# Kernel tuning notes

Hardware: AMD Instinct MI355X
Metric: run time of the kernel (lower is better)

The kernel has to match this reference:

```python
import jax, jax.numpy as jnp
import numpy as np
from functools import partial

INF = 1e10


def _softmin(a, b, c, gamma):
    # soft-min via -gamma * logsumexp(-x/gamma), numerically stable
    z = jnp.stack([a, b, c], axis=0) * (-1.0 / gamma)
    return -gamma * jax.nn.logsumexp(z, axis=0)


def rkd_sdtw(x, gamma):
    """Pairwise soft-DTW distances between all sequence pairs in the batch.

    x: [B, T, D] -> returns [B, B].
    """
    B, T, D = x.shape
    # pairwise squared-euclidean cost: C[a,b,t,s] = ||x[a,t]-x[b,s]||^2
    xn = jnp.sum(x * x, axis=-1)                      # [B, T]
    dot = jnp.einsum('atd,bsd->abts', x, x)           # [B, B, T, T]
    C = xn[:, None, :, None] + xn[None, :, None, :] - 2.0 * dot
    P = B * B
    C = C.reshape(P, T, T)

    idx = jnp.arange(T)

    def shift(r):  # r[i] -> r[i-1], pad INF at i=0
        return jnp.concatenate([jnp.full((P, 1), INF, r.dtype), r[:, :-1]], axis=1)

    def step(carry, d):
        r2, r1 = carry                                # diagonals d-2, d-1: [P, T]
        j = d - idx
        valid = (j >= 0) & (j < T)
        jc = jnp.clip(j, 0, T - 1)
        c_diag = C[:, idx, jc]                        # [P, T] cost on diagonal d
        up = shift(r1)        # R[i-1, j]
        left = r1             # R[i, j-1]
        diag = shift(r2)      # R[i-1, j-1]
        smin = _softmin(up, left, diag, gamma)
        smin = jnp.where(d == 0, 0.0, smin)           # R[0,0] = C[0,0]
        r = jnp.where(valid[None, :], c_diag + smin, INF)
        return (r1, r), None

    init = jnp.full((P, T), INF, C.dtype)
    (_, r_last), _ = jax.lax.scan(step, (init, init), jnp.arange(2 * T - 1))
    return r_last[:, T - 1].reshape(B, B)


def _smooth_l1(pred, target):
    d = pred - target
    ad = jnp.abs(d)
    return jnp.mean(jnp.where(ad < 1.0, 0.5 * d * d, ad - 0.5))


def setup_inputs() -> dict:
    key = jax.random.key(0)
    k1, k2 = jax.random.split(key)
    B, T, D = 32, 96, 128
    student = jax.random.normal(k1, (B, T, D), dtype=jnp.float32)
    teacher = jax.random.normal(k2, (B, T, D), dtype=jnp.float32)
    gamma = jnp.float32(1.0)
    return {"student": student, "teacher": teacher, "gamma": gamma}


def reference(student, teacher, gamma):
    # teacher branch computed under no_grad in torch -> stop_gradient here
    dtw_t = rkd_sdtw(teacher, gamma)
    dtw_t = dtw_t / jnp.mean(dtw_t)
    dtw_t = jax.lax.stop_gradient(dtw_t)

    dtw_s = rkd_sdtw(student, gamma)
    dtw_s = dtw_s / jnp.mean(dtw_s)
    return _smooth_l1(dtw_s, dtw_t)
```

## Files before the change

kernel.cpp:

```cpp
#include <hip/hip_runtime.h>


constexpr int TT = 96;
constexpr int DD = 128;
constexpr int BB = 32;
constexpr int NP = BB * BB;
constexpr int NPAIR = BB * (BB + 1) / 2;
constexpr int NPROB = 2 * NPAIR;
constexpr int CSZ = TT * TT;
constexpr float FINF = 1e10f;
constexpr float LOG2E = 1.4426950408889634f;
constexpr float LN2 = 0.6931471805599453f;

__device__ __forceinline__ int tri_base(int a) {
  return a * BB - (a * (a - 1)) / 2;
}
__device__ __forceinline__ void tri_decode(int pr, int& a, int& b) {
  a = (int)((65.0f - sqrtf(4225.0f - 8.0f * (float)pr)) * 0.5f);
  while (tri_base(a + 1) <= pr) ++a;
  while (tri_base(a) > pr) --a;
  b = a + (pr - tri_base(a));
}
__device__ __forceinline__ int diag_base(int d) {
  return (d <= 95) ? ((d * (d + 1)) >> 1)
                   : 4656 + (((d - 96) * (287 - d)) >> 1);
}
__device__ __forceinline__ float smin2(float u, float lf, float dg) {
  float m = fmaxf(fmaxf(u, lf), dg);
  float s = __builtin_amdgcn_exp2f(u - m) + __builtin_amdgcn_exp2f(lf - m)
          + __builtin_amdgcn_exp2f(dg - m);
  return m + __builtin_amdgcn_logf(s);
}

__global__ void xn_kernel(const float* __restrict__ xs,
                          const float* __restrict__ xt,
                          float* __restrict__ xn) {
  int idx = blockIdx.x * 256 + threadIdx.x;
  if (idx >= 2 * BB * TT) return;
  int which = idx / (BB * TT);
  int row = idx - which * (BB * TT);
  const float* x = which ? xt : xs;
  const float4* xv = reinterpret_cast<const float4*>(x + (size_t)row * DD);
  float acc = 0.f;
#pragma unroll
  for (int k = 0; k < DD / 4; ++k) {
    float4 v = xv[k];
    acc = fmaf(v.x, v.x, acc);
    acc = fmaf(v.y, v.y, acc);
    acc = fmaf(v.z, v.z, acc);
    acc = fmaf(v.w, v.w, acc);
  }
  xn[idx] = acc;
}

__global__ __launch_bounds__(256)
void csq_kernel(const float* __restrict__ xs,
                const float* __restrict__ xt,
                const float* __restrict__ xn,
                const float* __restrict__ gptr,
                float* __restrict__ Cd) {
  __shared__ __align__(16) float Cs[CSZ];
  __shared__ float xna[TT];
  __shared__ float xnb[TT];

  const int pr = blockIdx.x;
  int a, b;
  tri_decode(pr, a, b);
  const int w = blockIdx.y;
  const float* x = w ? xt : xs;
  const float* xnw = xn + w * (BB * TT);
  const float* xa = x + (size_t)a * TT * DD;
  const float* xb = x + (size_t)b * TT * DD;
  const int tid = threadIdx.x;

  if (tid < TT) {
    xna[tid] = xnw[a * TT + tid];
    xnb[tid] = xnw[b * TT + tid];
  }

  float4* sa = reinterpret_cast<float4*>(Cs);
  float4* sb = sa + TT * 9;

  const int wv = tid >> 6;
  const int lane = tid & 63;
  const int tx = (lane & 7) + (wv & 1) * 8;
  const int ty = (lane >> 3) + (wv >> 1) * 8;
  const int t0 = ty * 6, s0 = tx * 6;

  float acc[6][6];
#pragma unroll
  for (int r = 0; r < 6; ++r)
#pragma unroll
    for (int c = 0; c < 6; ++c) acc[r][c] = 0.f;

  const float4* ga = reinterpret_cast<const float4*>(xa);
  const float4* gb = reinterpret_cast<const float4*>(xb);

  for (int d0 = 0; d0 < 4; ++d0) {
    __syncthreads();
#pragma unroll
    for (int it = 0; it < 3; ++it) {
      int idx = tid + it * 256;
      int t = idx >> 3, k4 = idx & 7;
      int slot = (k4 + (t / 6)) & 7;
      sa[t * 9 + slot] = ga[t * 32 + d0 * 8 + k4];
      sb[t * 9 + slot] = gb[t * 32 + d0 * 8 + k4];
    }
    __syncthreads();
#pragma unroll
    for (int k4 = 0; k4 < 8; ++k4) {
      float4 av4[6], bv4[6];
      const int sA = (k4 + ty) & 7;
      const int sB = (k4 + tx) & 7;
#pragma unroll
      for (int r = 0; r < 6; ++r)
        av4[r] = sa[(t0 + r) * 9 + sA];
#pragma unroll
      for (int c = 0; c < 6; ++c)
        bv4[c] = sb[(s0 + c) * 9 + sB];
#pragma unroll
      for (int r = 0; r < 6; ++r)
#pragma unroll
        for (int c = 0; c < 6; ++c) {
          acc[r][c] = fmaf(av4[r].x, bv4[c].x, acc[r][c]);
          acc[r][c] = fmaf(av4[r].y, bv4[c].y, acc[r][c]);
          acc[r][c] = fmaf(av4[r].z, bv4[c].z, acc[r][c]);
          acc[r][c] = fmaf(av4[r].w, bv4[c].w, acc[r][c]);
        }
    }
  }
  __syncthreads();
  const float rg2 = -LOG2E / gptr[0];
#pragma unroll
  for (int r = 0; r < 6; ++r) {
    float xr = xna[t0 + r];
#pragma unroll
    for (int c = 0; c < 6; ++c) {
      float cv = xr + xnb[s0 + c] - 2.0f * acc[r][c];
      Cs[(t0 + r) * TT + (s0 + c)] = cv * rg2;
    }
  }
  __syncthreads();

  const size_t qb = (size_t)(w * NPAIR + pr) * CSZ;
  for (int d = wv; d < 2 * TT - 1; d += 4) {
    int s = d <= 95 ? 0 : d - 95;
    int len = d <= 95 ? d + 1 : 191 - d;
    int base = diag_base(d);
    if (lane < len) {
      int i = s + lane;
      Cd[qb + base + lane] = Cs[i * TT + (d - i)];
    }
    if (len > 64 && lane < len - 64) {
      int i = s + 64 + lane;
      Cd[qb + base + 64 + lane] = Cs[i * TT + (d - i)];
    }
  }
}

#define ST_R(d, qa, qb) do {                                             \
    float cA = qa, cB = qb;                                              \
    { int dn = (d) + 4;                                                  \
      if (dn <= 190) { int nb = diag_base(dn);                           \
        qa = cb[nb + l]; qb = cb[nb + 64 + l]; } }                       \
    float rA1 = __shfl(A1, lm1), rB1 = __shfl(B1, lm1);                  \
    float upA = l0 ? NEGI : rA1;                                         \
    float dgA = l0 ? NEGI : pA1;                                         \
    float upB = l0 ? rA1 : rB1;                                          \
    float dgB = l0 ? pA1 : pB1;                                          \
    float nA = cA + smin2(upA, A1, dgA);                                 \
    float nB = cB + smin2(upB, B1, dgB);                                 \
    A2 = A1; B2 = B1;                                                    \
    A1 = (l < (d) + 1) ? nA : NEGI;                                      \
    B1 = (64 + l < (d) + 1) ? nB : NEGI;                                 \
    pA1 = rA1; pB1 = rB1;                                                \
  } while (0)

#define ST_RN(d, qa, qb) do {       \
    float cA = qa;                                                       \
    { int dn = (d) + 4;                                                  \
      if (dn <= 190) { int nb = diag_base(dn);                           \
        qa = cb[nb + l]; qb = cb[nb + 64 + l]; } }                       \
    float rA1 = __shfl(A1, lm1);                                         \
    float upA = l0 ? NEGI : rA1;                                         \
    float dgA = l0 ? NEGI : pA1;                                         \
    float nA = cA + smin2(upA, A1, dgA);                                 \
    A2 = A1;                                                             \
    A1 = (l < (d) + 1) ? nA : NEGI;                                      \
    pA1 = rA1;                                                           \
  } while (0)

#define ST_F(d, qa, qb) do {                                             \
    float cA = qa, cB = qb;                                              \
    { int dn = (d) + 4;                                                  \
      if (dn <= 190) { int nb = diag_base(dn); qa = cb[nb + l];          \
        if (dn <= 128) qb = cb[nb + 64 + l]; } }                         \
    float rA1 = __shfl(A1, lp1), rB1 = __shfl(B1, lp1);                  \
    float lfA = l63 ? rB1 : rA1;                                         \
    float dgA = l63 ? pB1 : pA1;                                         \
    float nA = cA + smin2(A1, lfA, dgA);                                 \
    float nB = cB + smin2(B1, rB1, pB1);                                 \
    A1 = (l < 191 - (d)) ? nA : NEGI;                                    \
    B1 = (64 + l < 191 - (d)) ? nB : NEGI;                               \
    pA1 = rA1; pB1 = rB1;                                                \
  } while (0)

#define ST_FN(d, qa, qb) do {     \
    float cA = qa;                                                       \
    { int dn = (d) + 4;                                                  \
      if (dn <= 190) { int nb = diag_base(dn); qa = cb[nb + l]; } }      \
    float rA1 = __shfl(A1, lp1);                                         \
    float lfA = l63 ? NEGI : rA1;                                        \
    float dgA = l63 ? NEGI : pA1;                                        \
    float nA = cA + smin2(A1, lfA, dgA);                                 \
    A1 = (l < 191 - (d)) ? nA : NEGI;                                    \
    pA1 = rA1;                                                           \
  } while (0)

__global__ __launch_bounds__(64)
void dp_kernel(const float* __restrict__ Cd,
               const float* __restrict__ gptr,
               float* __restrict__ dtw) {
  const int q = blockIdx.x;
  const int l = threadIdx.x;
  const float gamma = gptr[0];
  const float rg2 = -LOG2E / gamma;
  const float NEGI = FINF * rg2;
  const float* __restrict__ cb = Cd + (size_t)q * CSZ;
  const int lp1 = (l + 1) & 63, lm1 = (l + 63) & 63;
  const bool l0 = (l == 0), l63 = (l == 63);

  float q0A, q0B, q1A, q1B, q2A, q2B, q3A, q3B;
  {
    int b1 = diag_base(1), b2 = diag_base(2), b3 = diag_base(3), b4 = diag_base(4);
    q0A = cb[b1 + l]; q0B = cb[b1 + 64 + l];
    q1A = cb[b2 + l]; q1B = cb[b2 + 64 + l];
    q2A = cb[b3 + l]; q2B = cb[b3 + 64 + l];
    q3A = cb[b4 + l]; q3B = cb[b4 + 64 + l];
  }

  float A1 = l0 ? cb[0] : NEGI;
  float B1 = NEGI, A2 = NEGI, B2 = NEGI;
  float pA1 = NEGI, pB1 = NEGI;

  for (int g = 0; g < 15; ++g) {
    int d = 1 + g * 4;
    ST_RN(d,     q0A, q0B);
    ST_RN(d + 1, q1A, q1B);
    ST_RN(d + 2, q2A, q2B);
    ST_RN(d + 3, q3A, q3B);
  }
  ST_RN(61, q0A, q0B);
  ST_RN(62, q1A, q1B);
  ST_RN(63, q2A, q2B);

  ST_R(64, q3A, q3B);
  for (int g = 0; g < 7; ++g) {
    int d = 65 + g * 4;
    ST_R(d,     q0A, q0B);
    ST_R(d + 1, q1A, q1B);
    ST_R(d + 2, q2A, q2B);
    ST_R(d + 3, q3A, q3B);
  }
  ST_R(93, q0A, q0B);
  ST_R(94, q1A, q1B);
  ST_R(95, q2A, q2B);

  {
    float cA = q3A, cB = q3B;
    int nb = diag_base(100);
    q3A = cb[nb + l]; q3B = cb[nb + 64 + l];
    float rA1 = __shfl(A1, lp1), rB1 = __shfl(B1, lp1);
    float lfA = l63 ? rB1 : rA1;
    float lfB = rB1;
    float nA = cA + smin2(A1, lfA, A2);
    float nB = cB + smin2(B1, lfB, B2);
    A1 = (l < 95) ? nA : NEGI;
    B1 = (64 + l < 95) ? nB : NEGI;
    pA1 = rA1; pB1 = rB1;
  }

  for (int g = 0; g < 8; ++g) {
    int d = 97 + g * 4;
    ST_F(d,     q0A, q0B);
    ST_F(d + 1, q1A, q1B);
    ST_F(d + 2, q2A, q2B);
    ST_F(d + 3, q3A, q3B);
  }
  for (int g = 0; g < 15; ++g) {
    int d = 129 + g * 4;
    ST_FN(d,     q0A, q0B);
    ST_FN(d + 1, q1A, q1B);
    ST_FN(d + 2, q2A, q2B);
    ST_FN(d + 3, q3A, q3B);
  }
  ST_FN(189, q0A, q0B);
  ST_FN(190, q1A, q1B);

  if (l0) {
    int w = q >= NPAIR ? 1 : 0;
    int pr = q - w * NPAIR;
    int a, b;
    tri_decode(pr, a, b);
    float v = A1 * (-gamma * LN2);
    dtw[w * NP + a * BB + b] = v;
    dtw[w * NP + b * BB + a] = v;
  }
}

__global__ __launch_bounds__(256)
void sdtw_fused_kernel(const float* __restrict__ xs,
                       const float* __restrict__ xt,
                       const float* __restrict__ xn,
                       const float* __restrict__ gptr,
                       float* __restrict__ dtw) {
  __shared__ __align__(16) float Cs[TT * TT];
  __shared__ float xna[TT];
  __shared__ float xnb[TT];

  const int pr = blockIdx.x;
  int a, b;
  tri_decode(pr, a, b);
  const int w = blockIdx.y;
  const float* x = w ? xt : xs;
  const float* xnw = xn + w * (BB * TT);
  const float* xa = x + (size_t)a * TT * DD;
  const float* xb = x + (size_t)b * TT * DD;
  const int tid = threadIdx.x;

  if (tid < TT) {
    xna[tid] = xnw[a * TT + tid];
    xnb[tid] = xnw[b * TT + tid];
  }
  constexpr int SROW = 36;
  float* xa_s = Cs;
  float* xb_s = Cs + TT * SROW;
  const int wv = tid >> 6;
  const int lane = tid & 63;
  const int tx = (lane & 7) + (wv & 1) * 8;
  const int ty = (lane >> 3) + (wv >> 1) * 8;
  const int t0 = ty * 6, s0 = tx * 6;
  float acc[6][6];
#pragma unroll
  for (int r = 0; r < 6; ++r)
#pragma unroll
    for (int c = 0; c < 6; ++c) acc[r][c] = 0.f;
  for (int d0 = 0; d0 < DD; d0 += 32) {
    __syncthreads();
    const float4* ga = reinterpret_cast<const float4*>(xa + d0);
    const float4* gb = reinterpret_cast<const float4*>(xb + d0);
    float4* sa = reinterpret_cast<float4*>(xa_s);
    float4* sb = reinterpret_cast<float4*>(xb_s);
#pragma unroll
    for (int it = 0; it < 3; ++it) {
      int idx = tid + it * 256;
      int t = idx >> 3, k4 = idx & 7;
      sa[t * (SROW / 4) + k4] = ga[t * (DD / 4) + k4];
      sb[t * (SROW / 4) + k4] = gb[t * (DD / 4) + k4];
    }
    __syncthreads();
#pragma unroll
    for (int k4 = 0; k4 < 8; ++k4) {
      float4 av4[6], bv4[6];
#pragma unroll
      for (int r = 0; r < 6; ++r)
        av4[r] = reinterpret_cast<const float4*>(xa_s + (t0 + r) * SROW)[k4];
#pragma unroll
      for (int c = 0; c < 6; ++c)
        bv4[c] = reinterpret_cast<const float4*>(xb_s + (s0 + c) * SROW)[k4];
#pragma unroll
      for (int r = 0; r < 6; ++r)
#pragma unroll
        for (int c = 0; c < 6; ++c) {
          acc[r][c] = fmaf(av4[r].x, bv4[c].x, acc[r][c]);
          acc[r][c] = fmaf(av4[r].y, bv4[c].y, acc[r][c]);
          acc[r][c] = fmaf(av4[r].z, bv4[c].z, acc[r][c]);
          acc[r][c] = fmaf(av4[r].w, bv4[c].w, acc[r][c]);
        }
    }
  }
  __syncthreads();
#pragma unroll
  for (int r = 0; r < 6; ++r) {
    float xr = xna[t0 + r];
#pragma unroll
    for (int c = 0; c < 6; ++c)
      Cs[(t0 + r) * TT + (s0 + c)] = xr + xnb[s0 + c] - 2.0f * acc[r][c];
  }
  __syncthreads();
  if (tid >= 64) return;

  const float gamma = gptr[0];
  const float rg = -1.0f / gamma;
  const int lm1 = (lane + 63) & 63;
  float A1 = FINF, B1 = FINF, A2 = FINF, B2 = FINF;
  for (int d = 0; d < 2 * TT - 1; ++d) {
    int jA = d - lane;
    bool vA = (jA >= 0) && (jA < TT);
    float cA = Cs[vA ? lane * TT + jA : 0];
    int iB = 64 + lane;
    int jB = d - iB;
    bool vB = (lane < 32) && (jB >= 0) && (jB < TT);
    float cB = Cs[vB ? iB * TT + jB : 0];
    float rA1 = __shfl(A1, lm1);
    float rB1 = __shfl(B1, lm1);
    float rA2 = __shfl(A2, lm1);
    float rB2 = __shfl(B2, lm1);
    const bool l0 = (lane == 0);
    float upA = l0 ? FINF : rA1;
    float dgA = l0 ? FINF : rA2;
    float upB = l0 ? rA1 : rB1;
    float dgB = l0 ? rA2 : rB2;
    float z0 = upA * rg, z1 = A1 * rg, z2 = dgA * rg;
    float m = fmaxf(fmaxf(z0, z1), z2);
    float s = expf(z0 - m) + expf(z1 - m) + expf(z2 - m);
    float sminA = -gamma * (m + logf(s));
    if (d == 0) sminA = 0.f;
    float y0 = upB * rg, y1 = B1 * rg, y2 = dgB * rg;
    float mb = fmaxf(fmaxf(y0, y1), y2);
    float sb2 = expf(y0 - mb) + expf(y1 - mb) + expf(y2 - mb);
    float sminB = -gamma * (mb + logf(sb2));
    float nA = vA ? cA + sminA : FINF;
    float nB = vB ? cB + sminB : FINF;
    A2 = A1; B2 = B1; A1 = nA; B1 = nB;
  }
  if (lane == 31) {
    float v = B1;
    dtw[w * NP + a * BB + b] = v;
    dtw[w * NP + b * BB + a] = v;
  }
}

__global__ void reduce_kernel(const float* __restrict__ dtw,
                              float* __restrict__ out) {
  __shared__ double sh[256];
  const int tid = threadIdx.x;
  double ss = 0, st = 0;
  for (int k = tid; k < NP; k += 256) {
    ss += (double)dtw[k];
    st += (double)dtw[NP + k];
  }
  sh[tid] = ss; __syncthreads();
  for (int o = 128; o > 0; o >>= 1) { if (tid < o) sh[tid] += sh[tid + o]; __syncthreads(); }
  double sum_s = sh[0]; __syncthreads();
  sh[tid] = st; __syncthreads();
  for (int o = 128; o > 0; o >>= 1) { if (tid < o) sh[tid] += sh[tid + o]; __syncthreads(); }
  double sum_t = sh[0]; __syncthreads();

  float mean_s = (float)(sum_s / NP);
  float mean_t = (float)(sum_t / NP);

  double acc = 0;
  for (int k = tid; k < NP; k += 256) {
    float pred = dtw[k] / mean_s;
    float targ = dtw[NP + k] / mean_t;
    float d = pred - targ;
    float ad = fabsf(d);
    float v = ad < 1.f ? 0.5f * d * d : ad - 0.5f;
    acc += (double)v;
  }
  sh[tid] = acc; __syncthreads();
  for (int o = 128; o > 0; o >>= 1) { if (tid < o) sh[tid] += sh[tid + o]; __syncthreads(); }
  if (tid == 0) out[0] = (float)(sh[0] / NP);
}

extern "C" void kernel_launch(void* const* d_in, const int* in_sizes, int n_in,
                              void* d_out, int out_size, void* d_ws, size_t ws_size,
                              hipStream_t stream) {
  const float* student = (const float*)d_in[0];
  const float* teacher = (const float*)d_in[1];
  const float* gamma   = (const float*)d_in[2];
  float* ws = (float*)d_ws;

  const size_t cd_floats = (size_t)NPROB * CSZ;
  const size_t need = (cd_floats + 2 * NP + 2 * BB * TT) * sizeof(float);

  if (ws_size >= need) {
    float* Cd  = ws;
    float* dtw = ws + cd_floats;
    float* xnb = dtw + 2 * NP;
    xn_kernel<<<24, 256, 0, stream>>>(student, teacher, xnb);
    csq_kernel<<<dim3(NPAIR, 2), 256, 0, stream>>>(student, teacher, xnb, gamma, Cd);
    dp_kernel<<<NPROB, 64, 0, stream>>>(Cd, gamma, dtw);
    reduce_kernel<<<1, 256, 0, stream>>>(dtw, (float*)d_out);
  } else {
    float* dtw = ws;
    float* xnb = ws + 2 * NP;
    xn_kernel<<<24, 256, 0, stream>>>(student, teacher, xnb);
    sdtw_fused_kernel<<<dim3(NPAIR, 2), 256, 0, stream>>>(student, teacher, xnb, gamma, dtw);
    reduce_kernel<<<1, 256, 0, stream>>>(dtw, (float*)d_out);
  }
}
```

Measured before the change: 93.22 us.

## Redundantly compute neighbor DP cells to move shuffles off the critical path

Each lane now also computes a ghost copy of its neighbor's cell on the anti-diagonal, loading the extra cost values. The shuffle that fetches the neighbor's value is issued after the update and consumed one step later, so cross-lane latency overlaps the next step's compute. In exchange the soft-min arithmetic and global loads per step roughly double, and the phase transitions get more complex bookkeeping.

```diff
diff --git a/kernel.cpp b/kernel.cpp
--- a/kernel.cpp
+++ b/kernel.cpp
@@ -158,63 +158,81 @@
   }
 }
 
-#define ST_R(d, qa, qb) do {                                             \
-    float cA = qa, cB = qb;                                              \
-    { int dn = (d) + 4;                                                  \
-      if (dn <= 190) { int nb = diag_base(dn);                           \
-        qa = cb[nb + l]; qb = cb[nb + 64 + l]; } }                       \
-    float rA1 = __shfl(A1, lm1), rB1 = __shfl(B1, lm1);                  \
-    float upA = l0 ? NEGI : rA1;                                         \
-    float dgA = l0 ? NEGI : pA1;                                         \
-    float upB = l0 ? rA1 : rB1;                                          \
-    float dgB = l0 ? pA1 : pB1;                                          \
-    float nA = cA + smin2(upA, A1, dgA);                                 \
-    float nB = cB + smin2(upB, B1, dgB);                                 \
-    A2 = A1; B2 = B1;                                                    \
-    A1 = (l < (d) + 1) ? nA : NEGI;                                      \
-    B1 = (64 + l < (d) + 1) ? nB : NEGI;                                 \
-    pA1 = rA1; pB1 = rB1;                                                \
+#define PREF(dn, sA, sG, sB, sH) do {                                    \
+    if ((dn) <= 190) {                                                   \
+      int nb = diag_base(dn);                                            \
+      int iA = nb + l;                 if (iA > CSZ - 1) iA = CSZ - 1;   \
+      sA = cb[iA];                                                       \
+      int iG = ((dn) <= 95) ? (nb + l - 1) : (nb + l + 1);               \
+      if (iG > CSZ - 1) iG = CSZ - 1;                                    \
+      sG = cb[iG];                                                       \
+      if ((dn) >= 63 && (dn) <= 128) {                                   \
+        int iB = nb + 64 + l;          if (iB > CSZ - 1) iB = CSZ - 1;   \
+        sB = cb[iB];                                                     \
+        int iH = ((dn) <= 95) ? (nb + 63 + l) : (nb + 65 + l);           \
+        if (iH > CSZ - 1) iH = CSZ - 1;                                  \
+        sH = cb[iH];                                                     \
+      }                                                                  \
+    }                                                                    \
   } while (0)
 
-#define ST_RN(d, qa, qb) do {       \
-    float cA = qa;                                                       \
-    { int dn = (d) + 4;                                                  \
-      if (dn <= 190) { int nb = diag_base(dn);                           \
-        qa = cb[nb + l]; qb = cb[nb + 64 + l]; } }                       \
-    float rA1 = __shfl(A1, lm1);                                         \
-    float upA = l0 ? NEGI : rA1;                                         \
-    float dgA = l0 ? NEGI : pA1;                                         \
-    float nA = cA + smin2(upA, A1, dgA);                                 \
-    A2 = A1;                                                             \
-    A1 = (l < (d) + 1) ? nA : NEGI;                                      \
-    pA1 = rA1;                                                           \
+#define GST_RN(d, sA, sG, sB, sH) do {       \
+    float cA = sA, cG = sG;                                              \
+    PREF((d) + 4, sA, sG, sB, sH);                                       \
+    float nA = cA + smin2(GA1, A1, GA2);                                 \
+    float nG = cG + smin2(hA, GA1, phA);                                 \
+    nA = (l <= (d)) ? nA : NEGI;                                         \
+    nG = (l >= 1 && l - 1 <= (d)) ? nG : NEGI;                           \
+    A2 = A1; GA2 = GA1; A1 = nA; GA1 = nG;                               \
+    phA = hA; hA = __shfl(GA1, lm1);                                     \
   } while (0)
 
-#define ST_F(d, qa, qb) do {                                             \
-    float cA = qa, cB = qb;                                              \
-    { int dn = (d) + 4;                                                  \
-      if (dn <= 190) { int nb = diag_base(dn); qa = cb[nb + l];          \
-        if (dn <= 128) qb = cb[nb + 64 + l]; } }                         \
-    float rA1 = __shfl(A1, lp1), rB1 = __shfl(B1, lp1);                  \
-    float lfA = l63 ? rB1 : rA1;                                         \
-    float dgA = l63 ? pB1 : pA1;                                         \
-    float nA = cA + smin2(A1, lfA, dgA);                                 \
-    float nB = cB + smin2(B1, rB1, pB1);                                 \
-    A1 = (l < 191 - (d)) ? nA : NEGI;                                    \
-    B1 = (64 + l < 191 - (d)) ? nB : NEGI;                               \
-    pA1 = rA1; pB1 = rB1;                                                \
+#define GST_RF(d, sA, sG, sB, sH) do {                 \
+    float cA = sA, cG = sG, cB = sB, cH = sH;                            \
+    PREF((d) + 4, sA, sG, sB, sH);                                       \
+    float nA = cA + smin2(GA1, A1, GA2);                                 \
+    float nB = cB + smin2(GB1, B1, GB2);                                 \
+    float nG = cG + smin2(hA, GA1, phA);                                 \
+    float hBe = l0 ? hA : hB, phBe = l0 ? phA : phB;                     \
+    float nH = cH + smin2(hBe, GB1, phBe);                               \
+    nA = (l <= (d)) ? nA : NEGI;                                         \
+    nB = (64 + l <= (d)) ? nB : NEGI;                                    \
+    nG = (l >= 1 && l - 1 <= (d)) ? nG : NEGI;                           \
+    nH = (63 + l <= (d)) ? nH : NEGI;                                    \
+    A2 = A1; B2 = B1; GA2 = GA1; GB2 = GB1;                              \
+    A1 = nA; B1 = nB; GA1 = nG; GB1 = nH;                                \
+    phA = hA; phB = hB;                                                  \
+    hA = __shfl(GA1, lm1); hB = __shfl(GB1, lm1);                        \
   } while (0)
 
-#define ST_FN(d, qa, qb) do {     \
-    float cA = qa;                                                       \
-    { int dn = (d) + 4;                                                  \
-      if (dn <= 190) { int nb = diag_base(dn); qa = cb[nb + l]; } }      \
-    float rA1 = __shfl(A1, lp1);                                         \
-    float lfA = l63 ? NEGI : rA1;                                        \
-    float dgA = l63 ? NEGI : pA1;                                        \
-    float nA = cA + smin2(A1, lfA, dgA);                                 \
-    A1 = (l < 191 - (d)) ? nA : NEGI;                                    \
-    pA1 = rA1;                                                           \
+#define GST_FF(d, sA, sG, sB, sH) do {                \
+    float cA = sA, cG = sG, cB = sB, cH = sH;                            \
+    PREF((d) + 4, sA, sG, sB, sH);                                       \
+    float nA = cA + smin2(A1, GA1, GA2);                                 \
+    float nB = cB + smin2(B1, GB1, GB2);                                 \
+    float hAe = l63 ? hB : hA, phAe = l63 ? phB : phA;                   \
+    float nG = cG + smin2(GA1, hAe, phAe);                               \
+    float nH = cH + smin2(GB1, hB, phB);                                 \
+    nA = (l < 191 - (d)) ? nA : NEGI;                                    \
+    nB = (64 + l < 191 - (d)) ? nB : NEGI;                               \
+    nG = (l + 1 < 191 - (d)) ? nG : NEGI;                                \
+    nH = (65 + l < 191 - (d)) ? nH : NEGI;                               \
+    GA2 = GA1; GB2 = GB1;                                                \
+    A1 = nA; B1 = nB; GA1 = nG; GB1 = nH;                                \
+    phA = hA; phB = hB;                                                  \
+    hA = __shfl(GA1, lp1); hB = __shfl(GB1, lp1);                        \
+  } while (0)
+
+#define GST_FN(d, sA, sG, sB, sH) do {     \
+    float cA = sA, cG = sG;                                              \
+    PREF((d) + 4, sA, sG, sB, sH);                                       \
+    float nA = cA + smin2(A1, GA1, GA2);                                 \
+    float hAe = l63 ? NEGI : hA, phAe = l63 ? NEGI : phA;                \
+    float nG = cG + smin2(GA1, hAe, phAe);                               \
+    nA = (l < 191 - (d)) ? nA : NEGI;                                    \
+    nG = (l + 1 < 191 - (d)) ? nG : NEGI;                                \
+    GA2 = GA1; A1 = nA; GA1 = nG;                                        \
+    phA = hA; hA = __shfl(GA1, lp1);                                     \
   } while (0)
 
 __global__ __launch_bounds__(64)
@@ -230,72 +248,83 @@
   const int lp1 = (l + 1) & 63, lm1 = (l + 63) & 63;
   const bool l0 = (l == 0), l63 = (l == 63);
 
-  float q0A, q0B, q1A, q1B, q2A, q2B, q3A, q3B;
-  {
-    int b1 = diag_base(1), b2 = diag_base(2), b3 = diag_base(3), b4 = diag_base(4);
-    q0A = cb[b1 + l]; q0B = cb[b1 + 64 + l];
-    q1A = cb[b2 + l]; q1B = cb[b2 + 64 + l];
-    q2A = cb[b3 + l]; q2B = cb[b3 + 64 + l];
-    q3A = cb[b4 + l]; q3B = cb[b4 + 64 + l];
-  }
+  float s0A = NEGI, s0G = NEGI, s0B = NEGI, s0H = NEGI;
+  float s1A = NEGI, s1G = NEGI, s1B = NEGI, s1H = NEGI;
+  float s2A = NEGI, s2G = NEGI, s2B = NEGI, s2H = NEGI;
+  float s3A = NEGI, s3G = NEGI, s3B = NEGI, s3H = NEGI;
+  PREF(1, s0A, s0G, s0B, s0H);
+  PREF(2, s1A, s1G, s1B, s1H);
+  PREF(3, s2A, s2G, s2B, s2H);
+  PREF(4, s3A, s3G, s3B, s3H);
 
   float A1 = l0 ? cb[0] : NEGI;
-  float B1 = NEGI, A2 = NEGI, B2 = NEGI;
-  float pA1 = NEGI, pB1 = NEGI;
+  float A2 = NEGI, B1 = NEGI, B2 = NEGI;
+  float GA1 = (l == 1) ? cb[0] : NEGI;
+  float GA2 = NEGI, GB1 = NEGI, GB2 = NEGI;
+  float hA = (l == 2) ? cb[0] : NEGI;
+  float hB = NEGI, phA = NEGI, phB = NEGI;
 
   for (int g = 0; g < 15; ++g) {
     int d = 1 + g * 4;
-    ST_RN(d,     q0A, q0B);
-    ST_RN(d + 1, q1A, q1B);
-    ST_RN(d + 2, q2A, q2B);
-    ST_RN(d + 3, q3A, q3B);
-  }
-  ST_RN(61, q0A, q0B);
-  ST_RN(62, q1A, q1B);
-  ST_RN(63, q2A, q2B);
-
-  ST_R(64, q3A, q3B);
+    GST_RN(d,     s0A, s0G, s0B, s0H);
+    GST_RN(d + 1, s1A, s1G, s1B, s1H);
+    GST_RN(d + 2, s2A, s2G, s2B, s2H);
+    GST_RN(d + 3, s3A, s3G, s3B, s3H);
+  }
+  GST_RN(61, s0A, s0G, s0B, s0H);
+  GST_RN(62, s1A, s1G, s1B, s1H);
+
+  GST_RF(63, s2A, s2G, s2B, s2H);
+  GST_RF(64, s3A, s3G, s3B, s3H);
   for (int g = 0; g < 7; ++g) {
     int d = 65 + g * 4;
-    ST_R(d,     q0A, q0B);
-    ST_R(d + 1, q1A, q1B);
-    ST_R(d + 2, q2A, q2B);
-    ST_R(d + 3, q3A, q3B);
-  }
-  ST_R(93, q0A, q0B);
-  ST_R(94, q1A, q1B);
-  ST_R(95, q2A, q2B);
+    GST_RF(d,     s0A, s0G, s0B, s0H);
+    GST_RF(d + 1, s1A, s1G, s1B, s1H);
+    GST_RF(d + 2, s2A, s2G, s2B, s2H);
+    GST_RF(d + 3, s3A, s3G, s3B, s3H);
+  }
+  GST_RF(93, s0A, s0G, s0B, s0H);
+  GST_RF(94, s1A, s1G, s1B, s1H);
+  GST_RF(95, s2A, s2G, s2B, s2H);
 
   {
-    float cA = q3A, cB = q3B;
-    int nb = diag_base(100);
-    q3A = cb[nb + l]; q3B = cb[nb + 64 + l];
+    float cA = s3A, cB = s3B;
+    PREF(100, s3A, s3G, s3B, s3H);
     float rA1 = __shfl(A1, lp1), rB1 = __shfl(B1, lp1);
     float lfA = l63 ? rB1 : rA1;
-    float lfB = rB1;
     float nA = cA + smin2(A1, lfA, A2);
-    float nB = cB + smin2(B1, lfB, B2);
-    A1 = (l < 95) ? nA : NEGI;
-    B1 = (64 + l < 95) ? nB : NEGI;
-    pA1 = rA1; pB1 = rB1;
+    float nB = cB + smin2(B1, rB1, B2);
+    nA = (l < 95) ? nA : NEGI;
+    nB = (64 + l < 95) ? nB : NEGI;
+    GA2 = lfA;
+    GB2 = (65 + l <= 95) ? rB1 : NEGI;
+    float rA1n = __shfl(nA, lp1), rB1n = __shfl(nB, lp1);
+    GA1 = l63 ? rB1n : rA1n;
+    GA1 = (l + 1 < 95) ? GA1 : NEGI;
+    GB1 = (65 + l < 95) ? rB1n : NEGI;
+    phA = __shfl(GA2, lp1);
+    phB = __shfl(GB2, lp1);
+    hA  = __shfl(GA1, lp1);
+    hB  = __shfl(GB1, lp1);
+    A1 = nA; B1 = nB;
   }
 
   for (int g = 0; g < 8; ++g) {
     int d = 97 + g * 4;
-    ST_F(d,     q0A, q0B);
-    ST_F(d + 1, q1A, q1B);
-    ST_F(d + 2, q2A, q2B);
-    ST_F(d + 3, q3A, q3B);
+    GST_FF(d,     s0A, s0G, s0B, s0H);
+    GST_FF(d + 1, s1A, s1G, s1B, s1H);
+    GST_FF(d + 2, s2A, s2G, s2B, s2H);
+    GST_FF(d + 3, s3A, s3G, s3B, s3H);
   }
   for (int g = 0; g < 15; ++g) {
     int d = 129 + g * 4;
-    ST_FN(d,     q0A, q0B);
-    ST_FN(d + 1, q1A, q1B);
-    ST_FN(d + 2, q2A, q2B);
-    ST_FN(d + 3, q3A, q3B);
-  }
-  ST_FN(189, q0A, q0B);
-  ST_FN(190, q1A, q1B);
+    GST_FN(d,     s0A, s0G, s0B, s0H);
+    GST_FN(d + 1, s1A, s1G, s1B, s1H);
+    GST_FN(d + 2, s2A, s2G, s2B, s2H);
+    GST_FN(d + 3, s3A, s3G, s3B, s3H);
+  }
+  GST_FN(189, s0A, s0G, s0B, s0H);
+  GST_FN(190, s1A, s1G, s1B, s1H);
 
   if (l0) {
     int w = q >= NPAIR ? 1 : 0;
```

Measured after the change: 106.5 us. +14.2%, slower.

## Process student and teacher DP problems together in one wavefront for ILP

Applied to the files above, without the earlier changes.

The soft-DTW DP kernel now runs both the student and the teacher problem for the same pair inside a single 64-lane wavefront, interleaving two independent recurrence chains. The grid shrinks from 1056 to 528 blocks. The goal is to hide shuffle and transcendental latency along the serial anti-diagonal chain by giving the scheduler two independent dependency chains. The cost is roughly double the register use and fewer wavefronts, which reduces parallelism across CUs.

```diff
diff --git a/kernel.cpp b/kernel.cpp
--- a/kernel.cpp
+++ b/kernel.cpp
@@ -158,153 +158,187 @@
   }
 }
 
-#define ST_R(d, qa, qb) do {                                             \
-    float cA = qa, cB = qb;                                              \
+#define ST_R2(d, qa0, qb0, qa1, qb1) do {                                \
+    float cA0 = qa0, cB0 = qb0, cA1 = qa1, cB1 = qb1;                    \
     { int dn = (d) + 4;                                                  \
       if (dn <= 190) { int nb = diag_base(dn);                           \
-        qa = cb[nb + l]; qb = cb[nb + 64 + l]; } }                       \
-    float rA1 = __shfl(A1, lm1), rB1 = __shfl(B1, lm1);                  \
-    float upA = l0 ? NEGI : rA1;                                         \
-    float dgA = l0 ? NEGI : pA1;                                         \
-    float upB = l0 ? rA1 : rB1;                                          \
-    float dgB = l0 ? pA1 : pB1;                                          \
-    float nA = cA + smin2(upA, A1, dgA);                                 \
-    float nB = cB + smin2(upB, B1, dgB);                                 \
-    A2 = A1; B2 = B1;                                                    \
-    A1 = (l < (d) + 1) ? nA : NEGI;                                      \
-    B1 = (64 + l < (d) + 1) ? nB : NEGI;                                 \
-    pA1 = rA1; pB1 = rB1;                                                \
+        qa0 = cb0[nb + l]; qb0 = cb0[nb + 64 + l];                       \
+        qa1 = cb1[nb + l]; qb1 = cb1[nb + 64 + l]; } }                   \
+    float rA10 = __shfl(A1_0, lm1), rB10 = __shfl(B1_0, lm1);            \
+    float rA11 = __shfl(A1_1, lm1), rB11 = __shfl(B1_1, lm1);            \
+    float upA0 = l0 ? NEGI : rA10, dgA0 = l0 ? NEGI : pA1_0;             \
+    float upB0 = l0 ? rA10 : rB10, dgB0 = l0 ? pA1_0 : pB1_0;            \
+    float upA1 = l0 ? NEGI : rA11, dgA1 = l0 ? NEGI : pA1_1;             \
+    float upB1 = l0 ? rA11 : rB11, dgB1 = l0 ? pA1_1 : pB1_1;            \
+    float nA0 = cA0 + smin2(upA0, A1_0, dgA0);                           \
+    float nB0 = cB0 + smin2(upB0, B1_0, dgB0);                           \
+    float nA1 = cA1 + smin2(upA1, A1_1, dgA1);                           \
+    float nB1 = cB1 + smin2(upB1, B1_1, dgB1);                           \
+    A2_0 = A1_0; B2_0 = B1_0; A2_1 = A1_1; B2_1 = B1_1;                  \
+    A1_0 = (l < (d) + 1) ? nA0 : NEGI;                                   \
+    B1_0 = (64 + l < (d) + 1) ? nB0 : NEGI;                              \
+    A1_1 = (l < (d) + 1) ? nA1 : NEGI;                                   \
+    B1_1 = (64 + l < (d) + 1) ? nB1 : NEGI;                              \
+    pA1_0 = rA10; pB1_0 = rB10; pA1_1 = rA11; pB1_1 = rB11;              \
   } while (0)
 
-#define ST_RN(d, qa, qb) do {       \
-    float cA = qa;                                                       \
+#define ST_RN2(d, qa0, qb0, qa1, qb1) do {   \
+    float cA0 = qa0, cA1 = qa1;                                          \
     { int dn = (d) + 4;                                                  \
       if (dn <= 190) { int nb = diag_base(dn);                           \
-        qa = cb[nb + l]; qb = cb[nb + 64 + l]; } }                       \
-    float rA1 = __shfl(A1, lm1);                                         \
-    float upA = l0 ? NEGI : rA1;                                         \
-    float dgA = l0 ? NEGI : pA1;                                         \
-    float nA = cA + smin2(upA, A1, dgA);                                 \
-    A2 = A1;                                                             \
-    A1 = (l < (d) + 1) ? nA : NEGI;                                      \
-    pA1 = rA1;                                                           \
+        qa0 = cb0[nb + l]; qb0 = cb0[nb + 64 + l];                       \
+        qa1 = cb1[nb + l]; qb1 = cb1[nb + 64 + l]; } }                   \
+    float rA10 = __shfl(A1_0, lm1), rA11 = __shfl(A1_1, lm1);            \
+    float upA0 = l0 ? NEGI : rA10, dgA0 = l0 ? NEGI : pA1_0;             \
+    float upA1 = l0 ? NEGI : rA11, dgA1 = l0 ? NEGI : pA1_1;             \
+    float nA0 = cA0 + smin2(upA0, A1_0, dgA0);                           \
+    float nA1 = cA1 + smin2(upA1, A1_1, dgA1);                           \
+    A2_0 = A1_0; A2_1 = A1_1;                                            \
+    A1_0 = (l < (d) + 1) ? nA0 : NEGI;                                   \
+    A1_1 = (l < (d) + 1) ? nA1 : NEGI;                                   \
+    pA1_0 = rA10; pA1_1 = rA11;                                          \
   } while (0)
 
-#define ST_F(d, qa, qb) do {                                             \
-    float cA = qa, cB = qb;                                              \
+#define ST_F2(d, qa0, qb0, qa1, qb1) do {             \
+    float cA0 = qa0, cB0 = qb0, cA1 = qa1, cB1 = qb1;                    \
     { int dn = (d) + 4;                                                  \
-      if (dn <= 190) { int nb = diag_base(dn); qa = cb[nb + l];          \
-        if (dn <= 128) qb = cb[nb + 64 + l]; } }                         \
-    float rA1 = __shfl(A1, lp1), rB1 = __shfl(B1, lp1);                  \
-    float lfA = l63 ? rB1 : rA1;                                         \
-    float dgA = l63 ? pB1 : pA1;                                         \
-    float nA = cA + smin2(A1, lfA, dgA);                                 \
-    float nB = cB + smin2(B1, rB1, pB1);                                 \
-    A1 = (l < 191 - (d)) ? nA : NEGI;                                    \
-    B1 = (64 + l < 191 - (d)) ? nB : NEGI;                               \
-    pA1 = rA1; pB1 = rB1;                                                \
+      if (dn <= 190) { int nb = diag_base(dn);                           \
+        qa0 = cb0[nb + l]; qa1 = cb1[nb + l];                            \
+        if (dn <= 128) { qb0 = cb0[nb + 64 + l]; qb1 = cb1[nb + 64 + l]; } } } \
+    float rA10 = __shfl(A1_0, lp1), rB10 = __shfl(B1_0, lp1);            \
+    float rA11 = __shfl(A1_1, lp1), rB11 = __shfl(B1_1, lp1);            \
+    float lfA0 = l63 ? rB10 : rA10, dgA0 = l63 ? pB1_0 : pA1_0;          \
+    float lfA1 = l63 ? rB11 : rA11, dgA1 = l63 ? pB1_1 : pA1_1;          \
+    float nA0 = cA0 + smin2(A1_0, lfA0, dgA0);                           \
+    float nB0 = cB0 + smin2(B1_0, rB10, pB1_0);                          \
+    float nA1 = cA1 + smin2(A1_1, lfA1, dgA1);                           \
+    float nB1 = cB1 + smin2(B1_1, rB11, pB1_1);                          \
+    A1_0 = (l < 191 - (d)) ? nA0 : NEGI;                                 \
+    B1_0 = (64 + l < 191 - (d)) ? nB0 : NEGI;                            \
+    A1_1 = (l < 191 - (d)) ? nA1 : NEGI;                                 \
+    B1_1 = (64 + l < 191 - (d)) ? nB1 : NEGI;                            \
+    pA1_0 = rA10; pB1_0 = rB10; pA1_1 = rA11; pB1_1 = rB11;              \
   } while (0)
 
-#define ST_FN(d, qa, qb) do {     \
-    float cA = qa;                                                       \
+#define ST_FN2(d, qa0, qb0, qa1, qb1) do {   \
+    float cA0 = qa0, cA1 = qa1;                                          \
     { int dn = (d) + 4;                                                  \
-      if (dn <= 190) { int nb = diag_base(dn); qa = cb[nb + l]; } }      \
-    float rA1 = __shfl(A1, lp1);                                         \
-    float lfA = l63 ? NEGI : rA1;                                        \
-    float dgA = l63 ? NEGI : pA1;                                        \
-    float nA = cA + smin2(A1, lfA, dgA);                                 \
-    A1 = (l < 191 - (d)) ? nA : NEGI;                                    \
-    pA1 = rA1;                                                           \
+      if (dn <= 190) { int nb = diag_base(dn);                           \
+        qa0 = cb0[nb + l]; qa1 = cb1[nb + l]; } }                        \
+    float rA10 = __shfl(A1_0, lp1), rA11 = __shfl(A1_1, lp1);            \
+    float lfA0 = l63 ? NEGI : rA10, dgA0 = l63 ? NEGI : pA1_0;           \
+    float lfA1 = l63 ? NEGI : rA11, dgA1 = l63 ? NEGI : pA1_1;           \
+    float nA0 = cA0 + smin2(A1_0, lfA0, dgA0);                           \
+    float nA1 = cA1 + smin2(A1_1, lfA1, dgA1);                           \
+    A1_0 = (l < 191 - (d)) ? nA0 : NEGI;                                 \
+    A1_1 = (l < 191 - (d)) ? nA1 : NEGI;                                 \
+    pA1_0 = rA10; pA1_1 = rA11;                                          \
   } while (0)
 
 __global__ __launch_bounds__(64)
 void dp_kernel(const float* __restrict__ Cd,
                const float* __restrict__ gptr,
                float* __restrict__ dtw) {
-  const int q = blockIdx.x;
+  const int pr = blockIdx.x;
   const int l = threadIdx.x;
   const float gamma = gptr[0];
   const float rg2 = -LOG2E / gamma;
   const float NEGI = FINF * rg2;
-  const float* __restrict__ cb = Cd + (size_t)q * CSZ;
+  const float* __restrict__ cb0 = Cd + (size_t)pr * CSZ;
+  const float* __restrict__ cb1 = Cd + (size_t)(NPAIR + pr) * CSZ;
   const int lp1 = (l + 1) & 63, lm1 = (l + 63) & 63;
   const bool l0 = (l == 0), l63 = (l == 63);
 
-  float q0A, q0B, q1A, q1B, q2A, q2B, q3A, q3B;
+  float q0A0, q0B0, q1A0, q1B0, q2A0, q2B0, q3A0, q3B0;
+  float q0A1, q0B1, q1A1, q1B1, q2A1, q2B1, q3A1, q3B1;
   {
     int b1 = diag_base(1), b2 = diag_base(2), b3 = diag_base(3), b4 = diag_base(4);
-    q0A = cb[b1 + l]; q0B = cb[b1 + 64 + l];
-    q1A = cb[b2 + l]; q1B = cb[b2 + 64 + l];
-    q2A = cb[b3 + l]; q2B = cb[b3 + 64 + l];
-    q3A = cb[b4 + l]; q3B = cb[b4 + 64 + l];
-  }
-
-  float A1 = l0 ? cb[0] : NEGI;
-  float B1 = NEGI, A2 = NEGI, B2 = NEGI;
-  float pA1 = NEGI, pB1 = NEGI;
+    q0A0 = cb0[b1 + l]; q0B0 = cb0[b1 + 64 + l];
+    q1A0 = cb0[b2 + l]; q1B0 = cb0[b2 + 64 + l];
+    q2A0 = cb0[b3 + l]; q2B0 = cb0[b3 + 64 + l];
+    q3A0 = cb0[b4 + l]; q3B0 = cb0[b4 + 64 + l];
+    q0A1 = cb1[b1 + l]; q0B1 = cb1[b1 + 64 + l];
+    q1A1 = cb1[b2 + l]; q1B1 = cb1[b2 + 64 + l];
+    q2A1 = cb1[b3 + l]; q2B1 = cb1[b3 + 64 + l];
+    q3A1 = cb1[b4 + l]; q3B1 = cb1[b4 + 64 + l];
+  }
+
+  float A1_0 = l0 ? cb0[0] : NEGI;
+  float A1_1 = l0 ? cb1[0] : NEGI;
+  float B1_0 = NEGI, A2_0 = NEGI, B2_0 = NEGI;
+  float B1_1 = NEGI, A2_1 = NEGI, B2_1 = NEGI;
+  float pA1_0 = NEGI, pB1_0 = NEGI;
+  float pA1_1 = NEGI, pB1_1 = NEGI;
 
   for (int g = 0; g < 15; ++g) {
     int d = 1 + g * 4;
-    ST_RN(d,     q0A, q0B);
-    ST_RN(d + 1, q1A, q1B);
-    ST_RN(d + 2, q2A, q2B);
-    ST_RN(d + 3, q3A, q3B);
-  }
-  ST_RN(61, q0A, q0B);
-  ST_RN(62, q1A, q1B);
-  ST_RN(63, q2A, q2B);
-
-  ST_R(64, q3A, q3B);
+    ST_RN2(d,     q0A0, q0B0, q0A1, q0B1);
+    ST_RN2(d + 1, q1A0, q1B0, q1A1, q1B1);
+    ST_RN2(d + 2, q2A0, q2B0, q2A1, q2B1);
+    ST_RN2(d + 3, q3A0, q3B0, q3A1, q3B1);
+  }
+  ST_RN2(61, q0A0, q0B0, q0A1, q0B1);
+  ST_RN2(62, q1A0, q1B0, q1A1, q1B1);
+  ST_RN2(63, q2A0, q2B0, q2A1, q2B1);
+
+  ST_R2(64, q3A0, q3B0, q3A1, q3B1);
   for (int g = 0; g < 7; ++g) {
     int d = 65 + g * 4;
-    ST_R(d,     q0A, q0B);
-    ST_R(d + 1, q1A, q1B);
-    ST_R(d + 2, q2A, q2B);
-    ST_R(d + 3, q3A, q3B);
-  }
-  ST_R(93, q0A, q0B);
-  ST_R(94, q1A, q1B);
-  ST_R(95, q2A, q2B);
+    ST_R2(d,     q0A0, q0B0, q0A1, q0B1);
+    ST_R2(d + 1, q1A0, q1B0, q1A1, q1B1);
+    ST_R2(d + 2, q2A0, q2B0, q2A1, q2B1);
+    ST_R2(d + 3, q3A0, q3B0, q3A1, q3B1);
+  }
+  ST_R2(93, q0A0, q0B0, q0A1, q0B1);
+  ST_R2(94, q1A0, q1B0, q1A1, q1B1);
+  ST_R2(95, q2A0, q2B0, q2A1, q2B1);
 
   {
-    float cA = q3A, cB = q3B;
+    float cA0 = q3A0, cB0 = q3B0, cA1 = q3A1, cB1 = q3B1;
     int nb = diag_base(100);
-    q3A = cb[nb + l]; q3B = cb[nb + 64 + l];
-    float rA1 = __shfl(A1, lp1), rB1 = __shfl(B1, lp1);
-    float lfA = l63 ? rB1 : rA1;
-    float lfB = rB1;
-    float nA = cA + smin2(A1, lfA, A2);
-    float nB = cB + smin2(B1, lfB, B2);
-    A1 = (l < 95) ? nA : NEGI;
-    B1 = (64 + l < 95) ? nB : NEGI;
-    pA1 = rA1; pB1 = rB1;
+    q3A0 = cb0[nb + l]; q3B0 = cb0[nb + 64 + l];
+    q3A1 = cb1[nb + l]; q3B1 = cb1[nb + 64 + l];
+    float rA10 = __shfl(A1_0, lp1), rB10 = __shfl(B1_0, lp1);
+    float rA11 = __shfl(A1_1, lp1), rB11 = __shfl(B1_1, lp1);
+    float lfA0 = l63 ? rB10 : rA10;
+    float lfA1 = l63 ? rB11 : rA11;
+    float nA0 = cA0 + smin2(A1_0, lfA0, A2_0);
+    float nB0 = cB0 + smin2(B1_0, rB10, B2_0);
+    float nA1 = cA1 + smin2(A1_1, lfA1, A2_1);
+    float nB1 = cB1 + smin2(B1_1, rB11, B2_1);
+    A1_0 = (l < 95) ? nA0 : NEGI;
+    B1_0 = (64 + l < 95) ? nB0 : NEGI;
+    A1_1 = (l < 95) ? nA1 : NEGI;
+    B1_1 = (64 + l < 95) ? nB1 : NEGI;
+    pA1_0 = rA10; pB1_0 = rB10; pA1_1 = rA11; pB1_1 = rB11;
   }
 
   for (int g = 0; g < 8; ++g) {
     int d = 97 + g * 4;
-    ST_F(d,     q0A, q0B);
-    ST_F(d + 1, q1A, q1B);
-    ST_F(d + 2, q2A, q2B);
-    ST_F(d + 3, q3A, q3B);
+    ST_F2(d,     q0A0, q0B0, q0A1, q0B1);
+    ST_F2(d + 1, q1A0, q1B0, q1A1, q1B1);
+    ST_F2(d + 2, q2A0, q2B0, q2A1, q2B1);
+    ST_F2(d + 3, q3A0, q3B0, q3A1, q3B1);
   }
   for (int g = 0; g < 15; ++g) {
     int d = 129 + g * 4;
-    ST_FN(d,     q0A, q0B);
-    ST_FN(d + 1, q1A, q1B);
-    ST_FN(d + 2, q2A, q2B);
-    ST_FN(d + 3, q3A, q3B);
-  }
-  ST_FN(189, q0A, q0B);
-  ST_FN(190, q1A, q1B);
+    ST_FN2(d,     q0A0, q0B0, q0A1, q0B1);
+    ST_FN2(d + 1, q1A0, q1B0, q1A1, q1B1);
+    ST_FN2(d + 2, q2A0, q2B0, q2A1, q2B1);
+    ST_FN2(d + 3, q3A0, q3B0, q3A1, q3B1);
+  }
+  ST_FN2(189, q0A0, q0B0, q0A1, q0B1);
+  ST_FN2(190, q1A0, q1B0, q1A1, q1B1);
 
   if (l0) {
-    int w = q >= NPAIR ? 1 : 0;
-    int pr = q - w * NPAIR;
     int a, b;
     tri_decode(pr, a, b);
-    float v = A1 * (-gamma * LN2);
-    dtw[w * NP + a * BB + b] = v;
-    dtw[w * NP + b * BB + a] = v;
+    float v0 = A1_0 * (-gamma * LN2);
+    float v1 = A1_1 * (-gamma * LN2);
+    dtw[a * BB + b] = v0;
+    dtw[b * BB + a] = v0;
+    dtw[NP + a * BB + b] = v1;
+    dtw[NP + b * BB + a] = v1;
   }
 }
 
@@ -481,7 +515,7 @@
     float* xnb = dtw + 2 * NP;
     xn_kernel<<<24, 256, 0, stream>>>(student, teacher, xnb);
     csq_kernel<<<dim3(NPAIR, 2), 256, 0, stream>>>(student, teacher, xnb, gamma, Cd);
-    dp_kernel<<<NPROB, 64, 0, stream>>>(Cd, gamma, dtw);
+    dp_kernel<<<NPAIR, 64, 0, stream>>>(Cd, gamma, dtw);
     reduce_kernel<<<1, 256, 0, stream>>>(dtw, (float*)d_out);
   } else {
     float* dtw = ws;
```

Result: slower. 105.1 us (+12.8%).
